# Kernel optimization log

Hardware: AMD Instinct MI355X
Metric: run time of the kernel (lower is better)

The kernel has to match this reference:

```python
import jax, jax.numpy as jnp
import numpy as np

B, S, D, H = 4, 2048, 1024, 16
HD = D // H


def setup_inputs() -> dict:
    key = jax.random.key(0)
    ks = jax.random.split(key, 11)
    s = 1.0 / np.sqrt(D)
    return {
        "query": jax.random.normal(ks[0], (B, S, D), jnp.float32),
        "key": jax.random.normal(ks[1], (B, S, D), jnp.float32),
        "value": jax.random.normal(ks[2], (B, S, D), jnp.float32),
        "Wq": jax.random.normal(ks[3], (D, D), jnp.float32) * s,
        "bq": jax.random.normal(ks[4], (D,), jnp.float32) * s,
        "Wk": jax.random.normal(ks[5], (D, D), jnp.float32) * s,
        "bk": jax.random.normal(ks[6], (D,), jnp.float32) * s,
        "Wv": jax.random.normal(ks[7], (D, D), jnp.float32) * s,
        "bv": jax.random.normal(ks[8], (D,), jnp.float32) * s,
        "Wo": jax.random.normal(ks[9], (D, D), jnp.float32) * s,
        "bo": jax.random.normal(ks[10], (D,), jnp.float32) * s,
    }


def reference(query, key, value, Wq, bq, Wk, bk, Wv, bv, Wo, bo):
    b = query.shape[0]
    # projections (torch Linear: x @ W.T + b)
    q = (query @ Wq.T + bq).reshape(b, -1, H, HD).transpose(0, 2, 1, 3)  # [B,H,S,hd]
    k = (key @ Wk.T + bk).reshape(b, -1, H, HD).transpose(0, 2, 1, 3)
    v = (value @ Wv.T + bv).reshape(b, -1, H, HD).transpose(0, 2, 1, 3)
    scores = jnp.einsum('bhqd,bhkd->bhqk', q, k) / jnp.sqrt(jnp.float32(HD))
    attn = jax.nn.softmax(scores, axis=-1)  # dropout = identity (eval)
    out = jnp.einsum('bhqk,bhkd->bhqd', attn, v)
    out = out.transpose(0, 2, 1, 3).reshape(b, -1, D)
    return out @ Wo.T + bo
```

## Files before the change

kernel.cpp:

```cpp
#include <hip/hip_runtime.h>
#include <stdint.h>

typedef __attribute__((ext_vector_type(8))) short  s16x8;
typedef __attribute__((ext_vector_type(4))) float  f32x4;
typedef __attribute__((ext_vector_type(4))) unsigned short u16x4;

__device__ __forceinline__ unsigned short f2bf(float f) {
  union { float f; uint32_t u; } x; x.f = f;
  uint32_t u = x.u;
  return (unsigned short)((u + 0x7fffu + ((u >> 16) & 1u)) >> 16);
}

__device__ __forceinline__ float fexp2(float x) {
  float r; asm("v_exp_f32 %0, %1" : "=v"(r) : "v"(x)); return r;
}
__device__ __forceinline__ uint32_t cvtpk_bf16(float lo, float hi) {
  uint32_t r; asm("v_cvt_pk_bf16_f32 %0, %1, %2" : "=v"(r) : "v"(lo), "v"(hi)); return r;
}

__device__ __forceinline__ void gload_lds16(const void* g, void* l) {
  __builtin_amdgcn_global_load_lds(
      (const __attribute__((address_space(1))) void*)g,
      (__attribute__((address_space(3))) void*)l, 16, 0, 0);
}

struct CvtJobs {
  const float* src[7];
  unsigned short* dst[7];
  int n4[7];
};
__global__ __launch_bounds__(256) void cvt_all(CvtJobs jobs) {
  const int j = blockIdx.y;
  const float* __restrict__ src = jobs.src[j];
  unsigned short* __restrict__ dst = jobs.dst[j];
  const int n4 = jobs.n4[j];
  const int stride = gridDim.x * blockDim.x;
  for (int i = blockIdx.x * blockDim.x + threadIdx.x; i < n4; i += stride) {
    f32x4 v = *(const f32x4*)(src + (size_t)i * 4);
    u16x4 o = { f2bf(v[0]), f2bf(v[1]), f2bf(v[2]), f2bf(v[3]) };
    *(u16x4*)(dst + (size_t)i * 4) = o;
  }
}

struct GemmJob {
  const unsigned short* A;
  const unsigned short* Bmat;
  const float* bias;
  unsigned short* C;
  int M, N, Nb;
  int bias_row;
  float scale;
};

__device__ __forceinline__ void gemm_core(const unsigned short* __restrict__ A,
                                          const unsigned short* __restrict__ Bw,
                                          int m0, int n0, int K,
                                          unsigned short* Al, unsigned short* Bl,
                                          f32x4 (&acc)[4][4]) {
  const int tid = threadIdx.x;
  const int l = tid & 63, w = tid >> 6;
  const int lr = l & 15, lc = l >> 4;
  const int wr = w >> 1, wc = w & 1;
  const int srow = l >> 2, skc = (l & 3) * 8;
  for (int kt = 0; kt < K; kt += 32) {
#pragma unroll
    for (int p = 0; p < 2; ++p) {
      int c = w + 4 * p;
      int row = c * 16 + srow;
      gload_lds16(A + (size_t)(m0 + row) * K + kt + skc, &Al[c * 512 + l * 8]);
      gload_lds16(Bw + (size_t)(n0 + row) * K + kt + skc, &Bl[c * 512 + l * 8]);
    }
    __syncthreads();
    s16x8 af[4], bfr[4];
#pragma unroll
    for (int i = 0; i < 4; ++i)
      af[i] = *(const s16x8*)&Al[(wr * 64 + i * 16 + lr) * 32 + lc * 8];
#pragma unroll
    for (int j = 0; j < 4; ++j)
      bfr[j] = *(const s16x8*)&Bl[(wc * 64 + j * 16 + lr) * 32 + lc * 8];
#pragma unroll
    for (int i = 0; i < 4; ++i)
#pragma unroll
      for (int j = 0; j < 4; ++j)
        acc[i][j] = __builtin_amdgcn_mfma_f32_16x16x32_bf16(af[i], bfr[j], acc[i][j], 0, 0, 0);
    __syncthreads();
  }
}

__global__ __launch_bounds__(256) void gemm_qkv(GemmJob j0, GemmJob j1, GemmJob j2) {
  __shared__ __align__(16) unsigned short Al[4096];
  __shared__ __align__(16) unsigned short Bl[4096];
  const GemmJob jb = (blockIdx.y == 0) ? j0 : (blockIdx.y == 1) ? j1 : j2;
  const int flat = blockIdx.x;
  const int m0 = (flat / jb.Nb) * 128, n0 = (flat % jb.Nb) * 128;
  f32x4 acc[4][4];
#pragma unroll
  for (int i = 0; i < 4; ++i)
#pragma unroll
    for (int j = 0; j < 4; ++j) acc[i][j] = (f32x4){0.f, 0.f, 0.f, 0.f};
  gemm_core(jb.A, jb.Bmat, m0, n0, 1024, Al, Bl, acc);
  const int tid = threadIdx.x;
  const int l = tid & 63, w = tid >> 6;
  const int lr = l & 15, lc = l >> 4;
  const int wr = w >> 1, wc = w & 1;
#pragma unroll
  for (int i = 0; i < 4; ++i) {
    const int row0 = m0 + wr * 64 + i * 16 + lc * 4;
    f32x4 brow;
    if (jb.bias_row) brow = *(const f32x4*)&jb.bias[row0];
#pragma unroll
    for (int j = 0; j < 4; ++j) {
      const int col = n0 + wc * 64 + j * 16 + lr;
      float bcol = jb.bias_row ? 0.f : jb.bias[col];
#pragma unroll
      for (int r = 0; r < 4; ++r) {
        float v = (acc[i][j][r] + (jb.bias_row ? brow[r] : bcol)) * jb.scale;
        jb.C[(size_t)(row0 + r) * jb.N + col] = f2bf(v);
      }
    }
  }
}

__global__ __launch_bounds__(256) void gemm_out(const unsigned short* __restrict__ A,
                                                const unsigned short* __restrict__ Bw,
                                                const float* __restrict__ bias,
                                                float* __restrict__ Cout,
                                                int M, int N, int K) {
  __shared__ __align__(16) unsigned short Al[4096];
  __shared__ __align__(16) unsigned short Bl[4096];
  const int m0 = blockIdx.x * 128, n0 = blockIdx.y * 128;
  f32x4 acc[4][4];
#pragma unroll
  for (int i = 0; i < 4; ++i)
#pragma unroll
    for (int j = 0; j < 4; ++j) acc[i][j] = (f32x4){0.f, 0.f, 0.f, 0.f};
  gemm_core(A, Bw, m0, n0, K, Al, Bl, acc);
  const int tid = threadIdx.x;
  const int l = tid & 63, w = tid >> 6;
  const int lr = l & 15, lc = l >> 4;
  const int wr = w >> 1, wc = w & 1;
#pragma unroll
  for (int i = 0; i < 4; ++i) {
    const int row0 = m0 + wr * 64 + i * 16 + lc * 4;
#pragma unroll
    for (int j = 0; j < 4; ++j) {
      const int col = n0 + wc * 64 + j * 16 + lr;
      float bcol = bias[col];
#pragma unroll
      for (int r = 0; r < 4; ++r)
        Cout[(size_t)(row0 + r) * N + col] = acc[i][j][r] + bcol;
    }
  }
}

__global__ __launch_bounds__(256) void attn_fwd(const unsigned short* __restrict__ qb,
                                                const unsigned short* __restrict__ kb,
                                                const unsigned short* __restrict__ vtb,
                                                unsigned short* __restrict__ ob) {
  __shared__ __align__(16) unsigned short Kl[2][4096];
  __shared__ __align__(16) unsigned short Vt[2][4096];
  const int tid = threadIdx.x;
  const int l = tid & 63, w = tid >> 6;
  const int lr = l & 15, lc = l >> 4;
  const int b = blockIdx.z, h = blockIdx.y;
  const int q0 = blockIdx.x * 64;
  const size_t qkbase = ((size_t)b * 2048) * 1024 + (size_t)h * 64;
  const size_t vtbase = (size_t)(h * 64) * 8192 + (size_t)b * 2048;

  s16x8 aq0, aq1;
  {
    const unsigned short* qp = qb + qkbase + (size_t)(q0 + w * 16 + lr) * 1024 + lc * 8;
    aq0 = *(const s16x8*)qp;
    aq1 = *(const s16x8*)(qp + 32);
  }

  float lsum = 0.f;
  f32x4 oacc[4];
#pragma unroll
  for (int nd = 0; nd < 4; ++nd) oacc[nd] = (f32x4){0.f, 0.f, 0.f, 0.f};

  const int rl = l >> 3;
  const int cs = (l & 7) ^ rl;
  const int rA = w * 16 + rl, rB = rA + 8;
#define RHO(rr) (8 * (((rr) >> 2) & 3) + 4 * (((rr) >> 4) & 1) + ((rr) & 3) + 32 * ((rr) >> 5))
  const unsigned short* ksrcA = kb + qkbase + (size_t)RHO(rA) * 1024 + cs * 8;
  const unsigned short* ksrcB = kb + qkbase + (size_t)RHO(rB) * 1024 + cs * 8;
#undef RHO
  const unsigned short* vsrc0 = vtb + vtbase + (size_t)rA * 8192 + cs * 8;
  const int dst0 = w * 2048 + l * 16;

#define STAGE(BUF, KV0) {                                                       \
    gload_lds16(ksrcA + (size_t)(KV0) * 1024, (char*)Kl[BUF] + dst0);           \
    gload_lds16(ksrcB + (size_t)(KV0) * 1024, (char*)Kl[BUF] + dst0 + 1024);    \
    gload_lds16(vsrc0 + (KV0),                (char*)Vt[BUF] + dst0);           \
    gload_lds16(vsrc0 + (KV0) + 65536,        (char*)Vt[BUF] + dst0 + 1024); }

  int off0[4];
#pragma unroll
  for (int ni = 0; ni < 4; ++ni)
    off0[ni] = (ni * 16 + lr) * 128 + ((lc ^ (lr & 7)) * 16);

  STAGE(0, 0);

  for (int t = 0; t < 32; ++t) {
    const int cur = t & 1;
    __syncthreads();
    if (t < 31) STAGE(cur ^ 1, (t + 1) * 64);

    f32x4 sf[4];
    __builtin_amdgcn_s_setprio(1);
#pragma unroll
    for (int ni = 0; ni < 4; ++ni) {
      s16x8 k0 = *(const s16x8*)((const char*)Kl[cur] + off0[ni]);
      s16x8 k1 = *(const s16x8*)((const char*)Kl[cur] + (off0[ni] ^ 64));
      f32x4 z = (f32x4){0.f, 0.f, 0.f, 0.f};
      z = __builtin_amdgcn_mfma_f32_16x16x32_bf16(k0, aq0, z, 0, 0, 0);
      z = __builtin_amdgcn_mfma_f32_16x16x32_bf16(k1, aq1, z, 0, 0, 0);
      sf[ni] = z;
    }
    __builtin_amdgcn_s_setprio(0);

    union { uint32_t u[4]; s16x8 v; } pa0u, pa1u;
#pragma unroll
    for (int ni = 0; ni < 4; ++ni) {
      float p0 = fexp2(sf[ni][0]);
      float p1 = fexp2(sf[ni][1]);
      float p2 = fexp2(sf[ni][2]);
      float p3 = fexp2(sf[ni][3]);
      lsum += (p0 + p1) + (p2 + p3);
      uint32_t w0 = cvtpk_bf16(p0, p1);
      uint32_t w1 = cvtpk_bf16(p2, p3);
      if (ni < 2) { pa0u.u[ni * 2] = w0; pa0u.u[ni * 2 + 1] = w1; }
      else        { pa1u.u[(ni - 2) * 2] = w0; pa1u.u[(ni - 2) * 2 + 1] = w1; }
    }

    __builtin_amdgcn_s_setprio(1);
#pragma unroll
    for (int nd = 0; nd < 4; ++nd) {
      s16x8 v0 = *(const s16x8*)((const char*)Vt[cur] + off0[nd]);
      s16x8 v1 = *(const s16x8*)((const char*)Vt[cur] + (off0[nd] ^ 64));
      oacc[nd] = __builtin_amdgcn_mfma_f32_16x16x32_bf16(pa0u.v, v0, oacc[nd], 0, 0, 0);
      oacc[nd] = __builtin_amdgcn_mfma_f32_16x16x32_bf16(pa1u.v, v1, oacc[nd], 0, 0, 0);
    }
    __builtin_amdgcn_s_setprio(0);
  }

  lsum += __shfl_xor(lsum, 16, 64);
  lsum += __shfl_xor(lsum, 32, 64);
  float linv[4];
#pragma unroll
  for (int r = 0; r < 4; ++r) linv[r] = 1.f / __shfl(lsum, lc * 4 + r, 64);
#pragma unroll
  for (int nd = 0; nd < 4; ++nd)
#pragma unroll
    for (int r = 0; r < 4; ++r) {
      int qrow = q0 + w * 16 + lc * 4 + r;
      ob[qkbase + (size_t)qrow * 1024 + nd * 16 + lr] = f2bf(oacc[nd][r] * linv[r]);
    }
#undef STAGE
}

extern "C" void kernel_launch(void* const* d_in, const int* in_sizes, int n_in,
                              void* d_out, int out_size, void* d_ws, size_t ws_size,
                              hipStream_t stream) {
  const float* query = (const float*)d_in[0];
  const float* key_  = (const float*)d_in[1];
  const float* value = (const float*)d_in[2];
  const float* Wq = (const float*)d_in[3];
  const float* bq = (const float*)d_in[4];
  const float* Wk = (const float*)d_in[5];
  const float* bk = (const float*)d_in[6];
  const float* Wv = (const float*)d_in[7];
  const float* bv = (const float*)d_in[8];
  const float* Wo = (const float*)d_in[9];
  const float* bo = (const float*)d_in[10];

  const int MS = 4 * 2048;
  const int D = 1024;
  const size_t NX = (size_t)MS * D;
  const size_t NW = (size_t)D * D;

  const size_t need = (6 * NX + 4 * NW) * 2;
  if (ws_size < need) return;

  unsigned short* ws  = (unsigned short*)d_ws;
  unsigned short* xq  = ws;
  unsigned short* xk  = xq + NX;
  unsigned short* xv  = xk + NX;
  unsigned short* qb_ = xv + NX;
  unsigned short* kb_ = qb_ + NX;
  unsigned short* vtb = kb_ + NX;
  unsigned short* wqb = vtb + NX;
  unsigned short* wkb = wqb + NW;
  unsigned short* wvb = wkb + NW;
  unsigned short* wob = wvb + NW;
  unsigned short* attn = xq;

  CvtJobs cj;
  cj.src[0] = query; cj.dst[0] = xq;  cj.n4[0] = (int)(NX / 4);
  cj.src[1] = key_;  cj.dst[1] = xk;  cj.n4[1] = (int)(NX / 4);
  cj.src[2] = value; cj.dst[2] = xv;  cj.n4[2] = (int)(NX / 4);
  cj.src[3] = Wq;    cj.dst[3] = wqb; cj.n4[3] = (int)(NW / 4);
  cj.src[4] = Wk;    cj.dst[4] = wkb; cj.n4[4] = (int)(NW / 4);
  cj.src[5] = Wv;    cj.dst[5] = wvb; cj.n4[5] = (int)(NW / 4);
  cj.src[6] = Wo;    cj.dst[6] = wob; cj.n4[6] = (int)(NW / 4);
  cvt_all<<<dim3(1024, 7), 256, 0, stream>>>(cj);

  const float qscale = 0.18033688f;
  GemmJob jq = { xq,  wqb, bq, qb_, MS, D,  D / 128,  0, qscale };
  GemmJob jk = { xk,  wkb, bk, kb_, MS, D,  D / 128,  0, 1.f };
  GemmJob jv = { wvb, xv,  bv, vtb, D,  MS, MS / 128, 1, 1.f };
  gemm_qkv<<<dim3(512, 3), 256, 0, stream>>>(jq, jk, jv);

  attn_fwd<<<dim3(2048 / 64, 16, 4), 256, 0, stream>>>(qb_, kb_, vtb, attn);

  gemm_out<<<dim3(MS / 128, D / 128), 256, 0, stream>>>(attn, wob, bo, (float*)d_out, MS, D, D);
}
```

Before: 233.5 us.

## Use 512-thread attention blocks with triple-buffered LDS and XCD-aware block remap

Each attention block now covers 128 query rows with 8 waves, so every staged K/V tile is shared by twice as many waves. Half the waves load K and half load V. The LDS ring grows from double to triple buffering, with explicit vmcnt waits and a raw s_barrier, so loads run two tiles ahead. A 1D grid with an XCD-interleaving remap groups blocks of the same head and batch together for cache locality. The risks are more LDS per block and lower occupancy, and correctness now depends on the hand-written waitcnt ordering.

Result: faster. 215.4 us (-7.7%).

```diff
diff --git a/kernel.cpp b/kernel.cpp
--- a/kernel.cpp
+++ b/kernel.cpp
@@ -153,17 +153,20 @@
   }
 }
 
-__global__ __launch_bounds__(256) void attn_fwd(const unsigned short* __restrict__ qb,
+__global__ __launch_bounds__(512) void attn_fwd(const unsigned short* __restrict__ qb,
                                                 const unsigned short* __restrict__ kb,
                                                 const unsigned short* __restrict__ vtb,
                                                 unsigned short* __restrict__ ob) {
-  __shared__ __align__(16) unsigned short Kl[2][4096];
-  __shared__ __align__(16) unsigned short Vt[2][4096];
+  __shared__ __align__(16) unsigned short L[3 * 8192];
   const int tid = threadIdx.x;
   const int l = tid & 63, w = tid >> 6;
   const int lr = l & 15, lc = l >> 4;
-  const int b = blockIdx.z, h = blockIdx.y;
-  const int q0 = blockIdx.x * 64;
+  const int i0 = blockIdx.x;
+  const int wid = (i0 & 7) * 128 + (i0 >> 3);
+  const int qx = wid & 15;
+  const int h = (wid >> 4) & 15;
+  const int b = wid >> 8;
+  const int q0 = qx * 128;
   const size_t qkbase = ((size_t)b * 2048) * 1024 + (size_t)h * 64;
   const size_t vtbase = (size_t)(h * 64) * 8192 + (size_t)b * 2048;
 
@@ -179,21 +182,29 @@
 #pragma unroll
   for (int nd = 0; nd < 4; ++nd) oacc[nd] = (f32x4){0.f, 0.f, 0.f, 0.f};
 
+  const int role = w >> 2, wk = w & 3;
   const int rl = l >> 3;
   const int cs = (l & 7) ^ rl;
-  const int rA = w * 16 + rl, rB = rA + 8;
+  const int rA = wk * 16 + rl, rB = rA + 8;
 #define RHO(rr) (8 * (((rr) >> 2) & 3) + 4 * (((rr) >> 4) & 1) + ((rr) & 3) + 32 * ((rr) >> 5))
-  const unsigned short* ksrcA = kb + qkbase + (size_t)RHO(rA) * 1024 + cs * 8;
-  const unsigned short* ksrcB = kb + qkbase + (size_t)RHO(rB) * 1024 + cs * 8;
+  const unsigned short* sA;
+  const unsigned short* sB;
+  size_t tstep;
+  if (role == 0) {
+    sA = kb + qkbase + (size_t)RHO(rA) * 1024 + cs * 8;
+    sB = kb + qkbase + (size_t)RHO(rB) * 1024 + cs * 8;
+    tstep = (size_t)64 * 1024;
+  } else {
+    sA = vtb + vtbase + (size_t)rA * 8192 + cs * 8;
+    sB = vtb + vtbase + (size_t)rB * 8192 + cs * 8;
+    tstep = 64;
+  }
 #undef RHO
-  const unsigned short* vsrc0 = vtb + vtbase + (size_t)rA * 8192 + cs * 8;
-  const int dst0 = w * 2048 + l * 16;
-
-#define STAGE(BUF, KV0) {                                                       \
-    gload_lds16(ksrcA + (size_t)(KV0) * 1024, (char*)Kl[BUF] + dst0);           \
-    gload_lds16(ksrcB + (size_t)(KV0) * 1024, (char*)Kl[BUF] + dst0 + 1024);    \
-    gload_lds16(vsrc0 + (KV0),                (char*)Vt[BUF] + dst0);           \
-    gload_lds16(vsrc0 + (KV0) + 65536,        (char*)Vt[BUF] + dst0 + 1024); }
+  char* dstL = (char*)L + role * 8192 + wk * 2048 + l * 16;
+
+#define STAGE(BUF, T) {                                              \
+    gload_lds16(sA + (size_t)(T) * tstep, dstL + (BUF) * 16384);     \
+    gload_lds16(sB + (size_t)(T) * tstep, dstL + (BUF) * 16384 + 1024); }
 
   int off0[4];
 #pragma unroll
@@ -201,18 +212,25 @@
     off0[ni] = (ni * 16 + lr) * 128 + ((lc ^ (lr & 7)) * 16);
 
   STAGE(0, 0);
-
+  STAGE(1, 1);
+
+  int cur = 0;
   for (int t = 0; t < 32; ++t) {
-    const int cur = t & 1;
-    __syncthreads();
-    if (t < 31) STAGE(cur ^ 1, (t + 1) * 64);
+    if (t < 31) asm volatile("s_waitcnt vmcnt(2)" ::: "memory");
+    else        asm volatile("s_waitcnt vmcnt(0)" ::: "memory");
+    __builtin_amdgcn_s_barrier();
+    if (t < 30) {
+      int nb = cur + 2; if (nb >= 3) nb -= 3;
+      STAGE(nb, t + 2);
+    }
+    const char* Lb = (const char*)L + cur * 16384;
 
     f32x4 sf[4];
     __builtin_amdgcn_s_setprio(1);
 #pragma unroll
     for (int ni = 0; ni < 4; ++ni) {
-      s16x8 k0 = *(const s16x8*)((const char*)Kl[cur] + off0[ni]);
-      s16x8 k1 = *(const s16x8*)((const char*)Kl[cur] + (off0[ni] ^ 64));
+      s16x8 k0 = *(const s16x8*)(Lb + off0[ni]);
+      s16x8 k1 = *(const s16x8*)(Lb + (off0[ni] ^ 64));
       f32x4 z = (f32x4){0.f, 0.f, 0.f, 0.f};
       z = __builtin_amdgcn_mfma_f32_16x16x32_bf16(k0, aq0, z, 0, 0, 0);
       z = __builtin_amdgcn_mfma_f32_16x16x32_bf16(k1, aq1, z, 0, 0, 0);
@@ -237,12 +255,14 @@
     __builtin_amdgcn_s_setprio(1);
 #pragma unroll
     for (int nd = 0; nd < 4; ++nd) {
-      s16x8 v0 = *(const s16x8*)((const char*)Vt[cur] + off0[nd]);
-      s16x8 v1 = *(const s16x8*)((const char*)Vt[cur] + (off0[nd] ^ 64));
+      s16x8 v0 = *(const s16x8*)(Lb + 8192 + off0[nd]);
+      s16x8 v1 = *(const s16x8*)(Lb + 8192 + (off0[nd] ^ 64));
       oacc[nd] = __builtin_amdgcn_mfma_f32_16x16x32_bf16(pa0u.v, v0, oacc[nd], 0, 0, 0);
       oacc[nd] = __builtin_amdgcn_mfma_f32_16x16x32_bf16(pa1u.v, v1, oacc[nd], 0, 0, 0);
     }
     __builtin_amdgcn_s_setprio(0);
+
+    ++cur; if (cur == 3) cur = 0;
   }
 
   lsum += __shfl_xor(lsum, 16, 64);
@@ -312,7 +332,7 @@
   GemmJob jv = { wvb, xv,  bv, vtb, D,  MS, MS / 128, 1, 1.f };
   gemm_qkv<<<dim3(512, 3), 256, 0, stream>>>(jq, jk, jv);
 
-  attn_fwd<<<dim3(2048 / 64, 16, 4), 256, 0, stream>>>(qb_, kb_, vtb, attn);
+  attn_fwd<<<dim3(1024), 512, 0, stream>>>(qb_, kb_, vtb, attn);
 
   gemm_out<<<dim3(MS / 128, D / 128), 256, 0, stream>>>(attn, wob, bo, (float*)d_out, MS, D, D);
 }
```
